# Kernel tuning notes

Hardware: AMD Instinct MI355X
Metric: run time of the kernel (lower is better)

## Reference

```python
import jax, jax.numpy as jnp
import numpy as np

B, S, HID = 1, 4096, 3584
NH, NKV, HD = 16, 8, 256
Q_SIZE, KV_SIZE = NH * HD, NKV * HD
SCALE = 256.0 ** -0.5          # query_pre_attn_scalar ** -0.5
SOFTCAP = 50.0                 # attn_logit_softcapping
WINDOW = 2048 - 1              # effective sliding window (sliding_window - 1)
THETA = 10000.0                # rope_theta
NEG = -1e30


def setup_inputs() -> dict:
    key = jax.random.key(0)
    k1, k2, k3 = jax.random.split(key, 3)
    hidden_states = jax.random.normal(k1, (B, S, HID), dtype=jnp.float32)
    position_ids = jnp.arange(S, dtype=jnp.int64).reshape(1, S)
    w_qkv = jax.random.normal(k2, (Q_SIZE + 2 * KV_SIZE, HID), dtype=jnp.float32) * 0.02
    w_o = jax.random.normal(k3, (HID, Q_SIZE), dtype=jnp.float32) * 0.02
    return {"position_ids": position_ids, "hidden_states": hidden_states,
            "w_qkv": w_qkv, "w_o": w_o}


def _rope_neox(x, pos):
    # x: [B, S, n_heads, HD]; pos: [B, S]
    half = HD // 2
    inv_freq = 1.0 / (THETA ** (jnp.arange(half, dtype=jnp.float32) * 2.0 / HD))
    ang = pos.astype(jnp.float32)[..., None] * inv_freq          # [B, S, half]
    cos = jnp.cos(ang)[:, :, None, :]                            # [B, S, 1, half]
    sin = jnp.sin(ang)[:, :, None, :]
    x1, x2 = x[..., :half], x[..., half:]
    return jnp.concatenate([x1 * cos - x2 * sin, x2 * cos + x1 * sin], axis=-1)


def reference(position_ids, hidden_states, w_qkv, w_o):
    # QKV projection (no bias)
    qkv = hidden_states @ w_qkv.T                                # [B, S, Q+2KV]
    q = qkv[..., :Q_SIZE].reshape(B, S, NH, HD)
    k = qkv[..., Q_SIZE:Q_SIZE + KV_SIZE].reshape(B, S, NKV, HD)
    v = qkv[..., Q_SIZE + KV_SIZE:].reshape(B, S, NKV, HD)

    # Neox-style RoPE over full head_dim
    q = _rope_neox(q, position_ids)
    k = _rope_neox(k, position_ids)

    # GQA: expand kv heads to query heads
    rep = NH // NKV
    k = jnp.repeat(k, rep, axis=2)                               # [B, S, NH, HD]
    v = jnp.repeat(v, rep, axis=2)

    # Scaled scores with tanh logit softcapping
    scores = jnp.einsum('bqhd,bkhd->bhqk', q, k) * SCALE
    scores = SOFTCAP * jnp.tanh(scores / SOFTCAP)

    # Causal + sliding-window mask: j <= i and i - j <= WINDOW
    i = jnp.arange(S)[:, None]
    j = jnp.arange(S)[None, :]
    mask = (j <= i) & (i - j <= WINDOW)                          # [S, S]
    scores = jnp.where(mask[None, None, :, :], scores, NEG)

    probs = jax.nn.softmax(scores, axis=-1)
    attn = jnp.einsum('bhqk,bkhd->bqhd', probs, v).reshape(B, S, Q_SIZE)

    # Output projection (no bias)
    return attn @ w_o.T                                          # [B, S, HID]
```

## Files before the change

kernel.cpp:

```cpp
#include <hip/hip_runtime.h>
#include <cstdint>
#include <cstddef>

#define S_LEN 4096
#define HID   3584
#define NH    16
#define NKV   8
#define HD    256
#define QSZ   (NH*HD)
#define KVSZ  (NKV*HD)
#define QKV_N (QSZ + 2*KVSZ)
#define WINDOW 2047

typedef unsigned short u16;
typedef __bf16 bf16x8 __attribute__((ext_vector_type(8)));
typedef u16    u16x8  __attribute__((ext_vector_type(8)));
typedef u16    u16x4  __attribute__((ext_vector_type(4)));
typedef float  f32x4  __attribute__((ext_vector_type(4)));

__device__ inline float bf2f(u16 u) {
    union { unsigned u; float f; } v; v.u = ((unsigned)u) << 16; return v.f;
}
__device__ inline u16 f2bf(float f) {
    union { float f; unsigned u; } v; v.f = f;
    return (u16)((v.u + 0x7FFF + ((v.u >> 16) & 1)) >> 16);
}
__device__ inline float fast_tanh(float x) {
    x = fminf(fmaxf(x, -20.f), 20.f);
    float e = __expf(2.f * x);
    return 1.f - 2.f / (e + 1.f);
}

typedef const __attribute__((address_space(1))) unsigned GU32;
typedef __attribute__((address_space(3))) unsigned LU32;
__device__ inline void gll16(const void* g, const void* l) {
    __builtin_amdgcn_global_load_lds((GU32*)(size_t)g,
                                     (LU32*)(unsigned)(size_t)l, 16, 0, 0);
}

__global__ __launch_bounds__(256)
void cast_f32_bf16(const float* __restrict__ src, u16* __restrict__ dst, int n4) {
    int i = blockIdx.x * blockDim.x + threadIdx.x;
    if (i >= n4) return;
    float4 v = ((const float4*)src)[i];
    u16x4 o;
    o[0] = f2bf(v.x); o[1] = f2bf(v.y); o[2] = f2bf(v.z); o[3] = f2bf(v.w);
    ((u16x4*)dst)[i] = o;
}

template<int BF16OUT>
__global__ __launch_bounds__(256)
void gemm_bt(const u16* __restrict__ A, const u16* __restrict__ B,
             void* __restrict__ Cv, int M, int N, int K) {
    __shared__ u16 lA[128 * 32];
    __shared__ u16 lB[128 * 32];
    const int tid  = threadIdx.x;
    const int lane = tid & 63, wave = tid >> 6;
    const int quad = lane >> 4, l16 = lane & 15;
    const int m0 = blockIdx.y * 128, n0 = blockIdx.x * 128;
    const int wm = (wave & 1) * 64, wn = (wave >> 1) * 64;

    f32x4 zero = {0.f, 0.f, 0.f, 0.f};
    f32x4 acc[4][4];
#pragma unroll
    for (int i = 0; i < 4; ++i)
#pragma unroll
        for (int j = 0; j < 4; ++j) acc[i][j] = zero;

    const int c0 = tid, c1 = tid + 256;
    const int r0 = c0 >> 2, cc0 = (c0 & 3) * 8;
    const int r1 = c1 >> 2, cc1 = (c1 & 3) * 8;
    const u16* A0 = A + (size_t)(m0 + r0) * K + cc0;
    const u16* A1 = A + (size_t)(m0 + r1) * K + cc1;
    const u16* B0 = B + (size_t)(n0 + r0) * K + cc0;
    const u16* B1 = B + (size_t)(n0 + r1) * K + cc1;

    u16x8 ra0 = *(const u16x8*)A0;
    u16x8 ra1 = *(const u16x8*)A1;
    u16x8 rb0 = *(const u16x8*)B0;
    u16x8 rb1 = *(const u16x8*)B1;

    for (int k0 = 0; k0 < K; k0 += 32) {
        __syncthreads();
        *(u16x8*)(&lA[c0 * 8]) = ra0;
        *(u16x8*)(&lA[c1 * 8]) = ra1;
        *(u16x8*)(&lB[c0 * 8]) = rb0;
        *(u16x8*)(&lB[c1 * 8]) = rb1;
        __syncthreads();
        int kn = k0 + 32;
        if (kn < K) {
            ra0 = *(const u16x8*)(A0 + kn);
            ra1 = *(const u16x8*)(A1 + kn);
            rb0 = *(const u16x8*)(B0 + kn);
            rb1 = *(const u16x8*)(B1 + kn);
        }
        bf16x8 af[4], bfr[4];
#pragma unroll
        for (int mt = 0; mt < 4; ++mt)
            af[mt] = *(const bf16x8*)(&lA[(wm + mt * 16 + l16) * 32 + quad * 8]);
#pragma unroll
        for (int nt = 0; nt < 4; ++nt)
            bfr[nt] = *(const bf16x8*)(&lB[(wn + nt * 16 + l16) * 32 + quad * 8]);
#pragma unroll
        for (int mt = 0; mt < 4; ++mt)
#pragma unroll
            for (int nt = 0; nt < 4; ++nt)
                acc[mt][nt] = __builtin_amdgcn_mfma_f32_16x16x32_bf16(
                    af[mt], bfr[nt], acc[mt][nt], 0, 0, 0);
    }

#pragma unroll
    for (int mt = 0; mt < 4; ++mt)
#pragma unroll
        for (int nt = 0; nt < 4; ++nt)
#pragma unroll
            for (int r = 0; r < 4; ++r) {
                int row = m0 + wm + mt * 16 + quad * 4 + r;
                int col = n0 + wn + nt * 16 + l16;
                float v = acc[mt][nt][r];
                if (BF16OUT) ((u16*)Cv)[(size_t)row * N + col] = f2bf(v);
                else         ((float*)Cv)[(size_t)row * N + col] = v;
            }
}

__global__ __launch_bounds__(256)
void rope_split(const u16* __restrict__ qkv, u16* __restrict__ Qb,
                u16* __restrict__ Kb) {
    const int s = blockIdx.x;
    const int t = threadIdx.x;
    const float pos = (float)s;
    const u16* row = qkv + (size_t)s * QKV_N;

    for (int p = t; p < 2048; p += 256) {
        int h = p >> 7, d = p & 127;
        float inv = __expf(-(float)d * 0.0719557841560639f);
        float ang = pos * inv, sn, cs;
        sincosf(ang, &sn, &cs);
        float x1 = bf2f(row[h * HD + d]);
        float x2 = bf2f(row[h * HD + d + 128]);
        size_t base = ((size_t)h * S_LEN + s) * HD;
        Qb[base + d]       = f2bf((x1 * cs - x2 * sn) * 0.0625f);
        Qb[base + d + 128] = f2bf((x2 * cs + x1 * sn) * 0.0625f);
    }
    for (int p = t; p < 1024; p += 256) {
        int h = p >> 7, d = p & 127;
        float inv = __expf(-(float)d * 0.0719557841560639f);
        float ang = pos * inv, sn, cs;
        sincosf(ang, &sn, &cs);
        float x1 = bf2f(row[QSZ + h * HD + d]);
        float x2 = bf2f(row[QSZ + h * HD + d + 128]);
        size_t base = ((size_t)h * S_LEN + s) * HD;
        Kb[base + d]       = f2bf(x1 * cs - x2 * sn);
        Kb[base + d + 128] = f2bf(x2 * cs + x1 * sn);
    }
}

__global__ __launch_bounds__(256)
void transpose_v(const u16* __restrict__ qkv, u16* __restrict__ Vt) {
    const int h = blockIdx.x, s0 = blockIdx.y * 64;
    const int tid = threadIdx.x;
    __shared__ u16 t[64 * 258];
    const u16* src = qkv + QSZ + KVSZ + (size_t)h * HD;
#pragma unroll
    for (int it = 0; it < 8; ++it) {
        int idx = it * 256 + tid;
        int sr = idx >> 5, c8 = (idx & 31) << 3;
        u16x8 v = *(const u16x8*)(src + (size_t)(s0 + sr) * QKV_N + c8);
#pragma unroll
        for (int j = 0; j < 8; ++j) t[sr * 258 + c8 + j] = v[j];
    }
    __syncthreads();
    const int lane = tid & 63, wave = tid >> 6;
    u16* dst = Vt + (size_t)h * HD * S_LEN + s0 + lane;
#pragma unroll
    for (int it = 0; it < 64; ++it) {
        int d = it * 4 + wave;
        dst[(size_t)d * S_LEN] = t[lane * 258 + d];
    }
}

__global__ __launch_bounds__(512)
void attn_fused(const u16* __restrict__ Qb, const u16* __restrict__ Kb,
                const u16* __restrict__ Vt, u16* __restrict__ O) {
    const int bid = blockIdx.x;
    const int hkv = bid & 7;
    const int qt  = bid >> 3;
    const int qbase = qt * 64;
    const int tid = threadIdx.x, wave = tid >> 6, lane = tid & 63;
    const int quad = lane >> 4, l16 = lane & 15;
    const int h  = hkv * 2 + (wave >> 2);
    const int qw = qbase + (wave & 3) * 16;

    __shared__ __align__(16) u16 lK[2][32 * 256];
    __shared__ __align__(16) u16 lV[2][32 * 256];
    __shared__ __align__(16) u16 lP[8][16 * 40];

    const int qrow = qw + l16;
    bf16x8 qf[8];
    {
        const u16* qp = Qb + ((size_t)h * S_LEN + qrow) * HD + quad * 8;
#pragma unroll
        for (int f = 0; f < 8; ++f) qf[f] = *(const bf16x8*)(qp + f * 32);
    }

    int koff[2], voff[2];
#pragma unroll
    for (int i = 0; i < 2; ++i) {
        int c = i * 512 + tid;
        int row = c >> 5, j = c & 31;
        koff[i] = row * 512 + ((j ^ (row & 7)) << 4);
        int d = c >> 2;
        int q = (c & 3) ^ ((d >> 1) & 3);
        voff[i] = d * (S_LEN * 2) + q * 16;
    }
    const char* Khb = (const char*)(Kb + (size_t)hkv * S_LEN * HD);
    const char* Vhb = (const char*)(Vt + (size_t)hkv * HD * S_LEN);

    const unsigned vrow = (unsigned)(l16 * 64)
                        + ((unsigned)(quad ^ ((l16 >> 1) & 3)) << 4);

    f32x4 zero = {0.f, 0.f, 0.f, 0.f};
    f32x4 o[16];
#pragma unroll
    for (int i = 0; i < 16; ++i) o[i] = zero;
    float m_r[4], l_r[4];
#pragma unroll
    for (int r = 0; r < 4; ++r) { m_r[r] = -1e4f; l_r[r] = 0.f; }

    const int t0 = max(0, qbase - WINDOW) >> 5;
    const int t1 = (qbase + 63) >> 5;

    auto stage = [&](int kb, int b) {
        const char* kp = Khb + ((size_t)kb << 9);
        const char* vp = Vhb + ((size_t)kb << 1);
#pragma unroll
        for (int i = 0; i < 2; ++i) {
            gll16(kp + koff[i], (const char*)&lK[b][0] + i * 8192 + wave * 1024);
            gll16(vp + voff[i], (const char*)&lV[b][0] + i * 8192 + wave * 1024);
        }
    };

    stage(t0 * 32, 0);
    asm volatile("s_waitcnt vmcnt(0)" ::: "memory");
    __syncthreads();

    int cur = 0;
    for (int kt = t0; kt <= t1; ++kt) {
        const int kb = kt * 32;
        if (kt < t1) stage((kt + 1) * 32, cur ^ 1);

        if ((kb <= qw + 15) && (kb + 31 >= qw - WINDOW)) {
            f32x4 sc[2];
            __builtin_amdgcn_s_setprio(1);
#pragma unroll
            for (int ct = 0; ct < 2; ++ct) {
                f32x4 a = zero;
                const char* kbase = (const char*)&lK[cur][0] + (ct * 16 + l16) * 512;
                const unsigned swz = (unsigned)((l16 & 7) << 4);
#pragma unroll
                for (int f = 0; f < 8; ++f) {
                    bf16x8 kf = *(const bf16x8*)(
                        kbase + (((unsigned)(f * 64 + quad * 16)) ^ swz));
                    a = __builtin_amdgcn_mfma_f32_16x16x32_bf16(qf[f], kf, a, 0, 0, 0);
                }
                sc[ct] = a;
            }
            __builtin_amdgcn_s_setprio(0);

            float p0[4], p1[4], rowmax[4];
#pragma unroll
            for (int r = 0; r < 4; ++r) {
                const int gi = qw + quad * 4 + r;
                float x0 = 50.f * fast_tanh(sc[0][r] * 0.02f);
                float x1 = 50.f * fast_tanh(sc[1][r] * 0.02f);
                int gj0 = kb + l16, gj1 = kb + 16 + l16;
                bool ok0 = (gj0 <= gi) && (gi - gj0 <= WINDOW);
                bool ok1 = (gj1 <= gi) && (gi - gj1 <= WINDOW);
                p0[r] = ok0 ? x0 : -1e30f;
                p1[r] = ok1 ? x1 : -1e30f;
                rowmax[r] = fmaxf(p0[r], p1[r]);
            }
#pragma unroll
            for (int m = 1; m < 16; m <<= 1)
#pragma unroll
                for (int r = 0; r < 4; ++r)
                    rowmax[r] = fmaxf(rowmax[r], __shfl_xor(rowmax[r], m, 64));

            float need = -1e30f;
#pragma unroll
            for (int r = 0; r < 4; ++r) need = fmaxf(need, rowmax[r] - m_r[r]);
            const bool upd = __any(need > 8.f) != 0;
            float al[4];
            if (upd) {
#pragma unroll
                for (int r = 0; r < 4; ++r) {
                    float mn = fmaxf(m_r[r], rowmax[r]);
                    al[r] = __expf(m_r[r] - mn);
                    m_r[r] = mn;
                }
            }

            float rs[4];
#pragma unroll
            for (int r = 0; r < 4; ++r) {
                p0[r] = __expf(p0[r] - m_r[r]);
                p1[r] = __expf(p1[r] - m_r[r]);
                rs[r] = p0[r] + p1[r];
            }
#pragma unroll
            for (int m = 1; m < 16; m <<= 1)
#pragma unroll
                for (int r = 0; r < 4; ++r)
                    rs[r] += __shfl_xor(rs[r], m, 64);

            if (upd) {
#pragma unroll
                for (int dt = 0; dt < 16; ++dt)
#pragma unroll
                    for (int r = 0; r < 4; ++r) o[dt][r] *= al[r];
#pragma unroll
                for (int r = 0; r < 4; ++r) l_r[r] = l_r[r] * al[r] + rs[r];
            } else {
#pragma unroll
                for (int r = 0; r < 4; ++r) l_r[r] += rs[r];
            }

            u16* pw = &lP[wave][0];
#pragma unroll
            for (int r = 0; r < 4; ++r) {
                pw[(quad * 4 + r) * 40 + l16]      = f2bf(p0[r]);
                pw[(quad * 4 + r) * 40 + 16 + l16] = f2bf(p1[r]);
            }
            asm volatile("s_waitcnt lgkmcnt(0)" ::: "memory");
            bf16x8 pf = *(const bf16x8*)(&pw[l16 * 40 + quad * 8]);

            __builtin_amdgcn_s_setprio(1);
#pragma unroll
            for (int dt = 0; dt < 16; ++dt) {
                bf16x8 vf = *(const bf16x8*)((const char*)&lV[cur][0] + dt * 1024 + vrow);
                o[dt] = __builtin_amdgcn_mfma_f32_16x16x32_bf16(pf, vf, o[dt], 0, 0, 0);
            }
            __builtin_amdgcn_s_setprio(0);
        }

        asm volatile("s_waitcnt vmcnt(0)" ::: "memory");
        __syncthreads();
        cur ^= 1;
    }

    float inv_l[4];
#pragma unroll
    for (int r = 0; r < 4; ++r) inv_l[r] = 1.f / l_r[r];
#pragma unroll
    for (int dt = 0; dt < 16; ++dt)
#pragma unroll
        for (int r = 0; r < 4; ++r) {
            int grow = qbase + (wave & 3) * 16 + quad * 4 + r;
            int gcol = h * HD + dt * 16 + l16;
            O[(size_t)grow * QSZ + gcol] = f2bf(o[dt][r] * inv_l[r]);
        }
}

extern "C" void kernel_launch(void* const* d_in, const int* in_sizes, int n_in,
                              void* d_out, int out_size, void* d_ws, size_t ws_size,
                              hipStream_t stream) {
    const float* hidden = (const float*)d_in[1];
    const float* w_qkv  = (const float*)d_in[2];
    const float* w_o    = (const float*)d_in[3];
    float* out = (float*)d_out;

    char* ws = (char*)d_ws;
    size_t off = 0;
    auto alloc = [&](size_t bytes) {
        void* p = ws + off; off += (bytes + 255) & ~(size_t)255; return p;
    };
    u16* Xb    = (u16*)alloc((size_t)S_LEN * HID   * 2);
    u16* Wqkvb = (u16*)alloc((size_t)QKV_N * HID   * 2);
    u16* QKVb  = (u16*)alloc((size_t)S_LEN * QKV_N * 2);
    u16* Qb    = (u16*)alloc((size_t)NH  * S_LEN * HD * 2);
    u16* Kb    = (u16*)alloc((size_t)NKV * S_LEN * HD * 2);
    u16* Vt    = (u16*)alloc((size_t)NKV * S_LEN * HD * 2);
    u16* attn  = QKVb;
    u16* Wob   = Xb;

    const int n1 = S_LEN * HID / 4;
    const int n2 = QKV_N * HID / 4;

    cast_f32_bf16<<<dim3((n1 + 255) / 256), dim3(256), 0, stream>>>(hidden, Xb, n1);
    cast_f32_bf16<<<dim3((n2 + 255) / 256), dim3(256), 0, stream>>>(w_qkv, Wqkvb, n2);
    gemm_bt<1><<<dim3(QKV_N / 128, S_LEN / 128), dim3(256), 0, stream>>>(
        Xb, Wqkvb, (void*)QKVb, S_LEN, QKV_N, HID);
    rope_split<<<dim3(S_LEN), dim3(256), 0, stream>>>(QKVb, Qb, Kb);
    transpose_v<<<dim3(NKV, S_LEN / 64), dim3(256), 0, stream>>>(QKVb, Vt);
    cast_f32_bf16<<<dim3((n1 + 255) / 256), dim3(256), 0, stream>>>(w_o, Wob, n1);
    attn_fused<<<dim3(512), dim3(512), 0, stream>>>(Qb, Kb, Vt, attn);
    gemm_bt<0><<<dim3(HID / 128, S_LEN / 128), dim3(256), 0, stream>>>(
        attn, Wob, (void*)out, S_LEN, HID, QSZ);
}
```

Before: 1.066 ms.

## Double-buffer GEMM via direct LDS loads and trim attention softmax overhead

```diff
diff --git a/kernel.cpp b/kernel.cpp
--- a/kernel.cpp
+++ b/kernel.cpp
@@ -25,10 +25,9 @@
     union { float f; unsigned u; } v; v.f = f;
     return (u16)((v.u + 0x7FFF + ((v.u >> 16) & 1)) >> 16);
 }
-__device__ inline float fast_tanh(float x) {
-    x = fminf(fmaxf(x, -20.f), 20.f);
-    float e = __expf(2.f * x);
-    return 1.f - 2.f / (e + 1.f);
+__device__ inline float softcap50(float s) {
+    float e = __expf(s * 0.04f);
+    return 50.f - 100.f / (e + 1.f);
 }
 
 typedef const __attribute__((address_space(1))) unsigned GU32;
@@ -52,8 +51,8 @@
 __global__ __launch_bounds__(256)
 void gemm_bt(const u16* __restrict__ A, const u16* __restrict__ B,
              void* __restrict__ Cv, int M, int N, int K) {
-    __shared__ u16 lA[128 * 32];
-    __shared__ u16 lB[128 * 32];
+    __shared__ u16 lA[2][128 * 32];
+    __shared__ u16 lB[2][128 * 32];
     const int tid  = threadIdx.x;
     const int lane = tid & 63, wave = tid >> 6;
     const int quad = lane >> 4, l16 = lane & 15;
@@ -68,45 +67,46 @@
         for (int j = 0; j < 4; ++j) acc[i][j] = zero;
 
     const int c0 = tid, c1 = tid + 256;
-    const int r0 = c0 >> 2, cc0 = (c0 & 3) * 8;
-    const int r1 = c1 >> 2, cc1 = (c1 & 3) * 8;
-    const u16* A0 = A + (size_t)(m0 + r0) * K + cc0;
-    const u16* A1 = A + (size_t)(m0 + r1) * K + cc1;
-    const u16* B0 = B + (size_t)(n0 + r0) * K + cc0;
-    const u16* B1 = B + (size_t)(n0 + r1) * K + cc1;
-
-    u16x8 ra0 = *(const u16x8*)A0;
-    u16x8 ra1 = *(const u16x8*)A1;
-    u16x8 rb0 = *(const u16x8*)B0;
-    u16x8 rb1 = *(const u16x8*)B1;
-
+    const u16* A0 = A + (size_t)(m0 + (c0 >> 2)) * K + (c0 & 3) * 8;
+    const u16* A1 = A + (size_t)(m0 + (c1 >> 2)) * K + (c1 & 3) * 8;
+    const u16* B0 = B + (size_t)(n0 + (c0 >> 2)) * K + (c0 & 3) * 8;
+    const u16* B1 = B + (size_t)(n0 + (c1 >> 2)) * K + (c1 & 3) * 8;
+    const int wb0 = wave * 1024, wb1 = 4096 + wave * 1024;
+
+    auto stage = [&](int k0, int b) {
+        gll16(A0 + k0, (const char*)&lA[b][0] + wb0);
+        gll16(A1 + k0, (const char*)&lA[b][0] + wb1);
+        gll16(B0 + k0, (const char*)&lB[b][0] + wb0);
+        gll16(B1 + k0, (const char*)&lB[b][0] + wb1);
+    };
+
+    stage(0, 0);
+    asm volatile("s_waitcnt vmcnt(0)" ::: "memory");
+    __syncthreads();
+
+    int cur = 0;
     for (int k0 = 0; k0 < K; k0 += 32) {
-        __syncthreads();
-        *(u16x8*)(&lA[c0 * 8]) = ra0;
-        *(u16x8*)(&lA[c1 * 8]) = ra1;
-        *(u16x8*)(&lB[c0 * 8]) = rb0;
-        *(u16x8*)(&lB[c1 * 8]) = rb1;
-        __syncthreads();
-        int kn = k0 + 32;
-        if (kn < K) {
-            ra0 = *(const u16x8*)(A0 + kn);
-            ra1 = *(const u16x8*)(A1 + kn);
-            rb0 = *(const u16x8*)(B0 + kn);
-            rb1 = *(const u16x8*)(B1 + kn);
-        }
+        if (k0 + 32 < K) stage(k0 + 32, cur ^ 1);
+
         bf16x8 af[4], bfr[4];
 #pragma unroll
         for (int mt = 0; mt < 4; ++mt)
-            af[mt] = *(const bf16x8*)(&lA[(wm + mt * 16 + l16) * 32 + quad * 8]);
+            af[mt] = *(const bf16x8*)(&lA[cur][(wm + mt * 16 + l16) * 32 + quad * 8]);
 #pragma unroll
         for (int nt = 0; nt < 4; ++nt)
-            bfr[nt] = *(const bf16x8*)(&lB[(wn + nt * 16 + l16) * 32 + quad * 8]);
+            bfr[nt] = *(const bf16x8*)(&lB[cur][(wn + nt * 16 + l16) * 32 + quad * 8]);
+        __builtin_amdgcn_s_setprio(1);
 #pragma unroll
         for (int mt = 0; mt < 4; ++mt)
 #pragma unroll
             for (int nt = 0; nt < 4; ++nt)
                 acc[mt][nt] = __builtin_amdgcn_mfma_f32_16x16x32_bf16(
                     af[mt], bfr[nt], acc[mt][nt], 0, 0, 0);
+        __builtin_amdgcn_s_setprio(0);
+
+        asm volatile("s_waitcnt vmcnt(0)" ::: "memory");
+        __syncthreads();
+        cur ^= 1;
     }
 
 #pragma unroll
@@ -195,10 +195,9 @@
     __shared__ __align__(16) u16 lV[2][32 * 256];
     __shared__ __align__(16) u16 lP[8][16 * 40];
 
-    const int qrow = qw + l16;
     bf16x8 qf[8];
     {
-        const u16* qp = Qb + ((size_t)h * S_LEN + qrow) * HD + quad * 8;
+        const u16* qp = Qb + ((size_t)h * S_LEN + qw + l16) * HD + quad * 8;
 #pragma unroll
         for (int f = 0; f < 8; ++f) qf[f] = *(const bf16x8*)(qp + f * 32);
     }
@@ -267,69 +266,71 @@
             }
             __builtin_amdgcn_s_setprio(0);
 
-            float p0[4], p1[4], rowmax[4];
-#pragma unroll
-            for (int r = 0; r < 4; ++r) {
-                const int gi = qw + quad * 4 + r;
-                float x0 = 50.f * fast_tanh(sc[0][r] * 0.02f);
-                float x1 = 50.f * fast_tanh(sc[1][r] * 0.02f);
-                int gj0 = kb + l16, gj1 = kb + 16 + l16;
-                bool ok0 = (gj0 <= gi) && (gi - gj0 <= WINDOW);
-                bool ok1 = (gj1 <= gi) && (gi - gj1 <= WINDOW);
-                p0[r] = ok0 ? x0 : -1e30f;
-                p1[r] = ok1 ? x1 : -1e30f;
-                rowmax[r] = fmaxf(p0[r], p1[r]);
-            }
-#pragma unroll
-            for (int m = 1; m < 16; m <<= 1)
-#pragma unroll
-                for (int r = 0; r < 4; ++r)
-                    rowmax[r] = fmaxf(rowmax[r], __shfl_xor(rowmax[r], m, 64));
+            float p0[4], p1[4];
+            const bool interior = (kb + 31 <= qw) && (kb + WINDOW >= qw + 15);
+            if (interior) {
+#pragma unroll
+                for (int r = 0; r < 4; ++r) {
+                    p0[r] = softcap50(sc[0][r]);
+                    p1[r] = softcap50(sc[1][r]);
+                }
+            } else {
+#pragma unroll
+                for (int r = 0; r < 4; ++r) {
+                    const int gi = qw + quad * 4 + r;
+                    float x0 = softcap50(sc[0][r]);
+                    float x1 = softcap50(sc[1][r]);
+                    int gj0 = kb + l16, gj1 = kb + 16 + l16;
+                    bool ok0 = (gj0 <= gi) && (gi - gj0 <= WINDOW);
+                    bool ok1 = (gj1 <= gi) && (gi - gj1 <= WINDOW);
+                    p0[r] = ok0 ? x0 : -1e30f;
+                    p1[r] = ok1 ? x1 : -1e30f;
+                }
+            }
 
             float need = -1e30f;
 #pragma unroll
-            for (int r = 0; r < 4; ++r) need = fmaxf(need, rowmax[r] - m_r[r]);
+            for (int r = 0; r < 4; ++r)
+                need = fmaxf(need, fmaxf(p0[r], p1[r]) - m_r[r]);
             const bool upd = __any(need > 8.f) != 0;
-            float al[4];
             if (upd) {
+                float rowmax[4];
+#pragma unroll
+                for (int r = 0; r < 4; ++r) rowmax[r] = fmaxf(p0[r], p1[r]);
+#pragma unroll
+                for (int m = 1; m < 16; m <<= 1)
+#pragma unroll
+                    for (int r = 0; r < 4; ++r)
+                        rowmax[r] = fmaxf(rowmax[r], __shfl_xor(rowmax[r], m, 64));
+                float al[4];
 #pragma unroll
                 for (int r = 0; r < 4; ++r) {
                     float mn = fmaxf(m_r[r], rowmax[r]);
                     al[r] = __expf(m_r[r] - mn);
                     m_r[r] = mn;
+                    l_r[r] *= al[r];
                 }
-            }
-
-            float rs[4];
+#pragma unroll
+                for (int dt = 0; dt < 16; ++dt)
+#pragma unroll
+                    for (int r = 0; r < 4; ++r) o[dt][r] *= al[r];
+            }
+
 #pragma unroll
             for (int r = 0; r < 4; ++r) {
                 p0[r] = __expf(p0[r] - m_r[r]);
                 p1[r] = __expf(p1[r] - m_r[r]);
-                rs[r] = p0[r] + p1[r];
-            }
-#pragma unroll
-            for (int m = 1; m < 16; m <<= 1)
-#pragma unroll
-                for (int r = 0; r < 4; ++r)
-                    rs[r] += __shfl_xor(rs[r], m, 64);
-
-            if (upd) {
-#pragma unroll
-                for (int dt = 0; dt < 16; ++dt)
-#pragma unroll
-                    for (int r = 0; r < 4; ++r) o[dt][r] *= al[r];
-#pragma unroll
-                for (int r = 0; r < 4; ++r) l_r[r] = l_r[r] * al[r] + rs[r];
-            } else {
-#pragma unroll
-                for (int r = 0; r < 4; ++r) l_r[r] += rs[r];
+                l_r[r] += p0[r] + p1[r];
             }
 
             u16* pw = &lP[wave][0];
 #pragma unroll
             for (int r = 0; r < 4; ++r) {
-                pw[(quad * 4 + r) * 40 + l16]      = f2bf(p0[r]);
-                pw[(quad * 4 + r) * 40 + 16 + l16] = f2bf(p1[r]);
+                unsigned pk;
+                asm("v_cvt_pk_bf16_f32 %0, %1, %2"
+                    : "=v"(pk) : "v"(p0[r]), "v"(p1[r]));
+                pw[(quad * 4 + r) * 40 + l16]      = (u16)pk;
+                pw[(quad * 4 + r) * 40 + 16 + l16] = (u16)(pk >> 16);
             }
             asm volatile("s_waitcnt lgkmcnt(0)" ::: "memory");
             bf16x8 pf = *(const bf16x8*)(&pw[l16 * 40 + quad * 8]);
@@ -348,6 +349,11 @@
         cur ^= 1;
     }
 
+#pragma unroll
+    for (int m = 1; m < 16; m <<= 1)
+#pragma unroll
+        for (int r = 0; r < 4; ++r)
+            l_r[r] += __shfl_xor(l_r[r], m, 64);
     float inv_l[4];
 #pragma unroll
     for (int r = 0; r < 4; ++r) inv_l[r] = 1.f / l_r[r];
```

After: 961.1 us. 1.11x faster.
